# Kernel tuning notes

Hardware: AMD Instinct MI355X
Metric: run time of the kernel (lower is better)

The kernel has to match this reference:

```python
import math
import jax, jax.numpy as jnp
import numpy as np

B, V, D, H, DE, DFF = 2, 2048, 1024, 16, 256, 4096
DK = D // H


def setup_inputs() -> dict:
    key = jax.random.key(0)
    ks = jax.random.split(key, 24)
    n = lambda k, shape, s=0.02: (jax.random.normal(k, shape, jnp.float32) * s)
    z = lambda *shape: jnp.zeros(shape, jnp.float32)
    return {
        'x': jax.random.normal(ks[0], (B, V, D), jnp.float32),
        'e_node': jax.random.normal(ks[1], (B, V, DE), jnp.float32),
        'conn': jax.random.uniform(ks[2], (B, V, V), jnp.float32),
        'ln1_g': jnp.ones((D,), jnp.float32), 'ln1_b': z(D),
        'f1w1': n(ks[3], (DE, 2 * D)), 'f1b1': z(2 * D),
        'f1w2': n(ks[4], (2 * D, 2 * D)), 'f1b2': z(2 * D),
        'wq': n(ks[5], (D, D)), 'bq': z(D),
        'wk': n(ks[6], (D, D)), 'bk': z(D),
        'wv': n(ks[7], (D, D)), 'bv': z(D),
        'wp': n(ks[8], (D, D)), 'bp': z(D),
        'ln2_g': jnp.ones((D,), jnp.float32), 'ln2_b': z(D),
        'f2w1': n(ks[9], (DE, 2 * D)), 'f2b1': z(2 * D),
        'f2w2': n(ks[10], (2 * D, 2 * D)), 'f2b2': z(2 * D),
        'ffw1': n(ks[11], (D, DFF)), 'ffb1': z(DFF),
        'ffw2': n(ks[12], (DFF, D)), 'ffb2': z(D),
    }


def _ln(x, g, b):
    m = x.mean(-1, keepdims=True)
    v = ((x - m) ** 2).mean(-1, keepdims=True)
    return (x - m) / jnp.sqrt(v + 1e-5) * g + b


def _film(e, w1, b1, w2, b2):
    h = jax.nn.gelu(e @ w1 + b1, approximate=False)  # torch F.gelu default = exact erf
    gb = h @ w2 + b2
    return jnp.split(gb, 2, axis=-1)  # gamma, beta


def reference(x, e_node, conn, ln1_g, ln1_b, f1w1, f1b1, f1w2, f1b2,
              wq, bq, wk, bk, wv, bv, wp, bp, ln2_g, ln2_b,
              f2w1, f2b1, f2w2, f2b2, ffw1, ffb1, ffw2, ffb2):
    b, v, d = x.shape
    # Pre-norm + FiLM 1
    y = _ln(x, ln1_g, ln1_b)
    g1, be1 = _film(e_node, f1w1, f1b1, f1w2, f1b2)
    y = y * (1.0 + g1) + be1
    # Multi-head attention with additive log(conn) mask
    heads = lambda t: t.reshape(b, v, H, DK).transpose(0, 2, 1, 3)  # [B,h,V,dk]
    Q = heads(y @ wq + bq)
    K = heads(y @ wk + bk)
    Vv = heads(y @ wv + bv)
    logits = jnp.einsum('bhqd,bhkd->bhqk', Q, K) / math.sqrt(DK)
    log_mask = jnp.log(jnp.clip(conn, 0.0, 1.0) + 1e-6)[:, None]  # [B,1,V,V]
    s = logits + log_mask
    s = s - s.max(-1, keepdims=True)
    a = jnp.exp(s)
    a = a / (a.sum(-1, keepdims=True) + 1e-8)
    o = jnp.einsum('bhqk,bhkd->bhqd', a, Vv)
    o = o.transpose(0, 2, 1, 3).reshape(b, v, d)
    x = x + (o @ wp + bp)
    # Pre-norm + FiLM 2 + FFN
    y2 = _ln(x, ln2_g, ln2_b)
    g2, be2 = _film(e_node, f2w1, f2b1, f2w2, f2b2)
    y2 = y2 * (1.0 + g2) + be2
    y2 = jax.nn.gelu(y2 @ ffw1 + ffb1, approximate=False) @ ffw2 + ffb2
    return x + y2
```

## Files before the change

### kernel.cpp

```cpp
#include <hip/hip_runtime.h>
#include <math.h>
#include <stdint.h>

#define B_   2
#define V_   2048
#define D_   1024
#define H_   16
#define DK_  64
#define DE_  256
#define DFF_ 4096
#define M_   (B_*V_)
#define D2_  (2*D_)
#define D3_  (3*D_)

typedef unsigned short u16;
typedef unsigned int   u32;
typedef __bf16 bf16x8 __attribute__((ext_vector_type(8)));
typedef u16    u16x8  __attribute__((ext_vector_type(8)));
typedef u16    u16x4  __attribute__((ext_vector_type(4)));
typedef float  f32x4  __attribute__((ext_vector_type(4)));
typedef u32    u32x2  __attribute__((ext_vector_type(2)));
typedef u32    u32x4  __attribute__((ext_vector_type(4)));

__device__ __forceinline__ float bf2f(u16 u) {
    union { unsigned int i; float f; } z; z.i = ((unsigned int)u) << 16; return z.f;
}
__device__ __forceinline__ u16 f2bf(float f) {
    union { float f; unsigned int i; } z; z.f = f;
    unsigned int x = z.i;
    return (u16)((x + 0x7fffu + ((x >> 16) & 1u)) >> 16);
}
__device__ __forceinline__ float gelu_erf(float v) {
    return 0.5f * v * (1.0f + erff(v * 0.70710678118654752f));
}
__device__ __forceinline__ float ldv(const float* p) { return *p; }
__device__ __forceinline__ float ldv(const u16* p)   { return bf2f(*p); }
__device__ __forceinline__ void  stv(float* p, float v) { *p = v; }
__device__ __forceinline__ void  stv(u16* p,   float v) { *p = f2bf(v); }

__device__ __forceinline__ void gload16(const u16* g, u16* lds)
{
    __builtin_amdgcn_global_load_lds(
        (const __attribute__((address_space(1))) void*)g,
        (__attribute__((address_space(3))) void*)(uintptr_t)lds,
        16, 0, 0);
}

__global__ void convT_k(const float* __restrict__ W, u16* __restrict__ Wt, int K, int N)
{
    __shared__ float tile[32][33];
    const int n0 = blockIdx.x * 32, k0 = blockIdx.y * 32;
    const int tx = threadIdx.x, ty = threadIdx.y;
    #pragma unroll
    for (int j = 0; j < 4; ++j)
        tile[ty * 4 + j][tx] = W[(size_t)(k0 + ty * 4 + j) * N + n0 + tx];
    __syncthreads();
    #pragma unroll
    for (int j = 0; j < 4; ++j)
        Wt[(size_t)(n0 + ty * 4 + j) * K + k0 + tx] = f2bf(tile[tx][ty * 4 + j]);
}

__global__ void conv_k(const float* __restrict__ X, u16* __restrict__ Y)
{
    const int i = (blockIdx.x * 256 + threadIdx.x) * 4;
    f32x4 v = *reinterpret_cast<const f32x4*>(X + i);
    u16x4 o;
    #pragma unroll
    for (int j = 0; j < 4; ++j) o[j] = f2bf(v[j]);
    *reinterpret_cast<u16x4*>(Y + i) = o;
}

__global__ void lmask_k(const float* __restrict__ conn, u16* __restrict__ Lm)
{
    const size_t i = ((size_t)blockIdx.x * 256 + threadIdx.x) * 8;
    f32x4 a = *reinterpret_cast<const f32x4*>(conn + i);
    f32x4 b = *reinterpret_cast<const f32x4*>(conn + i + 4);
    u16x8 o;
    #pragma unroll
    for (int j = 0; j < 4; ++j) {
        o[j]     = f2bf(__log2f(fminf(fmaxf(a[j], 0.f), 1.f) + 1e-6f));
        o[j + 4] = f2bf(__log2f(fminf(fmaxf(b[j], 0.f), 1.f) + 1e-6f));
    }
    *reinterpret_cast<u16x8*>(Lm + i) = o;
}

__global__ void qkvbias_k(const float* __restrict__ bq, const float* __restrict__ bk,
                          const float* __restrict__ bv, float* __restrict__ o)
{
    int i = blockIdx.x * 256 + threadIdx.x;
    o[i] = i < 1024 ? bq[i] : (i < 2048 ? bk[i - 1024] : bv[i - 2048]);
}

template<int EPI, int BN, typename TC, typename TRES>
__launch_bounds__(256)
__global__ void gemm_k(const u16* __restrict__ A, const u16* __restrict__ Wt,
                       const float* __restrict__ bias, const TRES* __restrict__ res,
                       TC* __restrict__ C, int M, int N, int K)
{
    constexpr int NB = BN / 32;
    constexpr int IB = BN / 32;
    __shared__ u16 As[128 * 64];
    __shared__ u16 Bs[BN * 64];

    const int tid  = threadIdx.x;
    const int lane = tid & 63;
    const int w    = tid >> 6;
    const int wm   = (w >> 1) * 64, wn = (w & 1) * (BN / 2);
    const int m0   = blockIdx.y * 128, n0 = blockIdx.x * BN;
    const int l15  = lane & 15, l4 = lane >> 4;
    const int rStage = lane >> 3;

    int rrA[4], ccA[4];
    #pragma unroll
    for (int i = 0; i < 4; ++i) {
        rrA[i] = w * 32 + i * 8 + rStage;
        ccA[i] = (lane & 7) ^ (rrA[i] & 7);
    }
    int rrB[IB], ccB[IB];
    #pragma unroll
    for (int i = 0; i < IB; ++i) {
        rrB[i] = w * (BN / 4) + i * 8 + rStage;
        ccB[i] = (lane & 7) ^ (rrB[i] & 7);
    }

    f32x4 acc[4][NB] = {};

    for (int k0 = 0; k0 < K; k0 += 64) {
        if (k0) __syncthreads();
        #pragma unroll
        for (int i = 0; i < 4; ++i)
            gload16(A + (size_t)(m0 + rrA[i]) * K + k0 + ccA[i] * 8, &As[w * 2048 + i * 512]);
        #pragma unroll
        for (int i = 0; i < IB; ++i)
            gload16(Wt + (size_t)(n0 + rrB[i]) * K + k0 + ccB[i] * 8, &Bs[w * (BN * 16) + i * 512]);
        __syncthreads();

        #pragma unroll
        for (int kk = 0; kk < 2; ++kk) {
            bf16x8 a[4], b[NB];
            #pragma unroll
            for (int mb = 0; mb < 4; ++mb) {
                int r  = wm + mb * 16 + l15;
                int ph = (kk * 4 + l4) ^ (r & 7);
                a[mb] = *reinterpret_cast<const bf16x8*>(&As[r * 64 + ph * 8]);
            }
            #pragma unroll
            for (int nb = 0; nb < NB; ++nb) {
                int r  = wn + nb * 16 + l15;
                int ph = (kk * 4 + l4) ^ (r & 7);
                b[nb] = *reinterpret_cast<const bf16x8*>(&Bs[r * 64 + ph * 8]);
            }
            #pragma unroll
            for (int mb = 0; mb < 4; ++mb)
                #pragma unroll
                for (int nb = 0; nb < NB; ++nb)
                    acc[mb][nb] = __builtin_amdgcn_mfma_f32_16x16x32_bf16(a[mb], b[nb], acc[mb][nb], 0, 0, 0);
        }
    }

    #pragma unroll
    for (int nb = 0; nb < NB; ++nb) {
        int col = n0 + wn + nb * 16 + l15;
        float bv = bias[col];
        #pragma unroll
        for (int mb = 0; mb < 4; ++mb) {
            #pragma unroll
            for (int i = 0; i < 4; ++i) {
                int row = m0 + wm + mb * 16 + l4 * 4 + i;
                float v = acc[mb][nb][i] + bv;
                if (EPI == 1) v = gelu_erf(v);
                if (EPI == 2) v += ldv(res + (size_t)row * N + col);
                stv(C + (size_t)row * N + col, v);
            }
        }
    }
}

template<int EPI, typename TC>
__launch_bounds__(512, 2)
__global__ void gemm256_k(const u16* __restrict__ A, const u16* __restrict__ Wt,
                          const float* __restrict__ bias,
                          TC* __restrict__ C, int M, int N, int K)
{
    __shared__ u16 As[2][256 * 64];
    __shared__ u16 Bs[2][256 * 64];

    const int tid  = threadIdx.x;
    const int lane = tid & 63;
    const int w    = tid >> 6;
    const int wm   = (w >> 2) * 128;
    const int wn   = (w & 3) * 64;
    const int m0   = blockIdx.y * 256, n0 = blockIdx.x * 256;
    const int l15  = lane & 15, l4 = lane >> 4;

    int rr[4], cc[4];
    #pragma unroll
    for (int i = 0; i < 4; ++i) {
        rr[i] = i * 64 + w * 8 + (lane >> 3);
        cc[i] = (lane & 7) ^ (rr[i] & 7);
    }

    f32x4 acc[8][4] = {};
    const int NT = K / 64;

    #pragma unroll
    for (int i = 0; i < 4; ++i) {
        gload16(A  + (size_t)(m0 + rr[i]) * K + cc[i] * 8, &As[0][i * 4096 + w * 512]);
        gload16(Wt + (size_t)(n0 + rr[i]) * K + cc[i] * 8, &Bs[0][i * 4096 + w * 512]);
    }

    for (int t = 0; t < NT; ++t) {
        const int d = t & 1;
        __syncthreads();

        if (t + 1 < NT) {
            const int k1 = (t + 1) * 64;
            #pragma unroll
            for (int i = 0; i < 4; ++i) {
                gload16(A  + (size_t)(m0 + rr[i]) * K + k1 + cc[i] * 8, &As[d ^ 1][i * 4096 + w * 512]);
                gload16(Wt + (size_t)(n0 + rr[i]) * K + k1 + cc[i] * 8, &Bs[d ^ 1][i * 4096 + w * 512]);
            }
        }

        #pragma unroll
        for (int ph = 0; ph < 4; ++ph) {
            const int mh = ph >> 1, nh = ph & 1;
            bf16x8 a[4][2], b[2][2];
            #pragma unroll
            for (int mf = 0; mf < 4; ++mf)
                #pragma unroll
                for (int kk = 0; kk < 2; ++kk) {
                    int r  = wm + (mh * 4 + mf) * 16 + l15;
                    int p2 = (kk * 4 + l4) ^ (r & 7);
                    a[mf][kk] = *reinterpret_cast<const bf16x8*>(&As[d][r * 64 + p2 * 8]);
                }
            #pragma unroll
            for (int nf = 0; nf < 2; ++nf)
                #pragma unroll
                for (int kk = 0; kk < 2; ++kk) {
                    int r  = wn + (nh * 2 + nf) * 16 + l15;
                    int p2 = (kk * 4 + l4) ^ (r & 7);
                    b[nf][kk] = *reinterpret_cast<const bf16x8*>(&Bs[d][r * 64 + p2 * 8]);
                }
            __builtin_amdgcn_s_setprio(1);
            #pragma unroll
            for (int mf = 0; mf < 4; ++mf)
                #pragma unroll
                for (int nf = 0; nf < 2; ++nf)
                    #pragma unroll
                    for (int kk = 0; kk < 2; ++kk)
                        acc[mh * 4 + mf][nh * 2 + nf] = __builtin_amdgcn_mfma_f32_16x16x32_bf16(
                            a[mf][kk], b[nf][kk], acc[mh * 4 + mf][nh * 2 + nf], 0, 0, 0);
            __builtin_amdgcn_s_setprio(0);
            __builtin_amdgcn_sched_barrier(0);
        }
    }

    #pragma unroll
    for (int nf = 0; nf < 4; ++nf) {
        int col = n0 + wn + nf * 16 + l15;
        float bv = bias[col];
        #pragma unroll
        for (int mf = 0; mf < 8; ++mf) {
            #pragma unroll
            for (int i = 0; i < 4; ++i) {
                int row = m0 + wm + mf * 16 + l4 * 4 + i;
                float v = acc[mf][nf][i] + bv;
                if (EPI == 1) v = gelu_erf(v);
                stv(C + (size_t)row * N + col, v);
            }
        }
    }
}

template<typename TX>
__launch_bounds__(256)
__global__ void lnfilm_k(const TX* __restrict__ X, const u16* __restrict__ GB,
                         const float* __restrict__ g, const float* __restrict__ bb,
                         u16* __restrict__ Y)
{
    const int row = blockIdx.x;
    const int tid = threadIdx.x;
    const int d0  = tid * 4;
    const TX* xr = X + (size_t)row * D_ + d0;
    float xs[4], s = 0.f, sq = 0.f;
    if constexpr (sizeof(TX) == 4) {
        f32x4 v4 = *reinterpret_cast<const f32x4*>(xr);
        #pragma unroll
        for (int j = 0; j < 4; ++j) { xs[j] = v4[j]; s += xs[j]; sq += xs[j] * xs[j]; }
    } else {
        u16x4 v4 = *reinterpret_cast<const u16x4*>(xr);
        #pragma unroll
        for (int j = 0; j < 4; ++j) { xs[j] = bf2f(v4[j]); s += xs[j]; sq += xs[j] * xs[j]; }
    }
    #pragma unroll
    for (int off = 32; off; off >>= 1) {
        s  += __shfl_xor(s, off);
        sq += __shfl_xor(sq, off);
    }
    __shared__ float rs[4], rq[4];
    const int w = tid >> 6;
    if ((tid & 63) == 0) { rs[w] = s; rq[w] = sq; }
    __syncthreads();
    s  = rs[0] + rs[1] + rs[2] + rs[3];
    sq = rq[0] + rq[1] + rq[2] + rq[3];
    const float mean = s * (1.0f / D_);
    const float var  = sq * (1.0f / D_) - mean * mean;
    const float rstd = rsqrtf(fmaxf(var, 0.f) + 1e-5f);
    const u16* gbr = GB + (size_t)row * D2_ + d0;
    u16x4 g4 = *reinterpret_cast<const u16x4*>(gbr);
    u16x4 b4 = *reinterpret_cast<const u16x4*>(gbr + D_);
    f32x4 gg = *reinterpret_cast<const f32x4*>(g + d0);
    f32x4 bv = *reinterpret_cast<const f32x4*>(bb + d0);
    u16x4 o;
    #pragma unroll
    for (int j = 0; j < 4; ++j) {
        float v = (xs[j] - mean) * rstd * gg[j] + bv[j];
        v = v * (1.0f + bf2f(g4[j])) + bf2f(b4[j]);
        o[j] = f2bf(v);
    }
    *reinterpret_cast<u16x4*>(Y + (size_t)row * D_ + d0) = o;
}

__launch_bounds__(256)
__global__ void attn_k(const u16* __restrict__ Q, const u16* __restrict__ K,
                       const u16* __restrict__ Vv, const u16* __restrict__ Lm,
                       u16* __restrict__ O, int ld)
{
    __shared__ u16 Ks[64 * 64];
    __shared__ u16 Vs[64 * 64];
    __shared__ u16 Lms[128 * 64];
    __shared__ u16 Ps[128 * 72];

    const int blk = blockIdx.x;
    const int qt  = blk & 15;
    const int h   = (blk >> 4) & 15;
    const int b   = blk >> 8;
    const int q0  = qt * 128;
    const int tid = threadIdx.x, lane = tid & 63, w = tid >> 6;
    const int l15 = lane & 15, l4 = lane >> 4;
    const size_t bV = (size_t)b * V_;

    bf16x8 qa[2][2];
    #pragma unroll
    for (int g = 0; g < 2; ++g) {
        const u16* qp = Q + (bV + q0 + w * 32 + g * 16 + l15) * ld + h * 64;
        u16x8 r0 = *reinterpret_cast<const u16x8*>(qp + l4 * 8);
        u16x8 r1 = *reinterpret_cast<const u16x8*>(qp + 32 + l4 * 8);
        u16x8 s0, s1;
        #pragma unroll
        for (int j = 0; j < 8; ++j) {
            s0[j] = f2bf(bf2f(r0[j]) * 0.125f);
            s1[j] = f2bf(bf2f(r1[j]) * 0.125f);
        }
        union { u16x8 u; bf16x8 h; } c0, c1;
        c0.u = s0; c1.u = s1;
        qa[g][0] = c0.h; qa[g][1] = c1.h;
    }

    const int rStage = (lane >> 3);
    const int cSw    = ((lane & 7) ^ rStage) * 8;
    const int vK     = ((lane >> 5) << 2) + ((lane & 7) >> 1);
    const int vDk    = ((lane >> 3) & 3) * 16 + (lane & 1) * 8;
    const u32 vaddr  = (u32)(uintptr_t)&Vs[0] + (l4 << 10) + (l15 << 3);

    int lmOff[4];
    #pragma unroll
    for (int kb = 0; kb < 4; ++kb)
        lmOff[kb] = ((((kb << 1) | (l4 >> 1)) ^ (l15 & 7)) << 3);

    const float LOG2E = 1.44269504088896f;
    float lrp[2] = {0.f, 0.f};
    f32x4 o4[2][4] = {};

    for (int kt = 0; kt < V_ / 64; ++kt) {
        const int k0 = kt * 64;
        if (kt) __syncthreads();
        #pragma unroll
        for (int i = 0; i < 2; ++i) {
            int r  = i * 32 + w * 8 + rStage;
            int kv = i * 32 + w * 8 + vK;
            gload16(K  + (bV + k0 + r)  * ld + h * 64 + cSw, &Ks[i * 2048 + w * 512]);
            gload16(Vv + (bV + k0 + kv) * ld + h * 64 + vDk, &Vs[i * 2048 + w * 512]);
        }
        #pragma unroll
        for (int i = 0; i < 4; ++i) {
            int r = i * 32 + w * 8 + rStage;
            gload16(Lm + (bV + q0 + r) * (size_t)V_ + k0 + cSw, &Lms[i * 2048 + w * 512]);
        }
        __syncthreads();

        #pragma unroll
        for (int g = 0; g < 2; ++g) {
            f32x4 s[4];
            #pragma unroll
            for (int kb = 0; kb < 4; ++kb) {
                int row = (kb * 16 + l15) * 64;
                bf16x8 k0f = *reinterpret_cast<const bf16x8*>(&Ks[row + ((l4 ^ (l15 & 7)) * 8)]);
                bf16x8 k1f = *reinterpret_cast<const bf16x8*>(&Ks[row + (((l4 + 4) ^ (l15 & 7)) * 8)]);
                f32x4 z = {};
                __builtin_amdgcn_s_setprio(1);
                z = __builtin_amdgcn_mfma_f32_16x16x32_bf16(k0f, qa[g][0], z, 0, 0, 0);
                z = __builtin_amdgcn_mfma_f32_16x16x32_bf16(k1f, qa[g][1], z, 0, 0, 0);
                __builtin_amdgcn_s_setprio(0);
                s[kb] = z;
            }
            const int lmRow = w * 32 + g * 16 + l15;
            const u16* lmBase = &Lms[lmRow * 64 + (l4 & 1) * 4];
            u16* psW = &Ps[lmRow * 72 + l4 * 4];
            #pragma unroll
            for (int kb = 0; kb < 4; ++kb) {
                u16x4 lm4 = *reinterpret_cast<const u16x4*>(lmBase + lmOff[kb]);
                float p0, p1, p2, p3;
                float t0 = fmaf(s[kb][0], LOG2E, bf2f(lm4[0]));
                float t1 = fmaf(s[kb][1], LOG2E, bf2f(lm4[1]));
                float t2 = fmaf(s[kb][2], LOG2E, bf2f(lm4[2]));
                float t3 = fmaf(s[kb][3], LOG2E, bf2f(lm4[3]));
                asm("v_exp_f32 %0, %1" : "=v"(p0) : "v"(t0));
                asm("v_exp_f32 %0, %1" : "=v"(p1) : "v"(t1));
                asm("v_exp_f32 %0, %1" : "=v"(p2) : "v"(t2));
                asm("v_exp_f32 %0, %1" : "=v"(p3) : "v"(t3));
                lrp[g] += (p0 + p1) + (p2 + p3);
                u32 d0, d1;
                asm("v_cvt_pk_bf16_f32 %0, %1, %2" : "=v"(d0) : "v"(p0), "v"(p1));
                asm("v_cvt_pk_bf16_f32 %0, %1, %2" : "=v"(d1) : "v"(p2), "v"(p3));
                u32x2 dd = {d0, d1};
                *reinterpret_cast<u32x2*>(psW + kb * 16) = dd;
            }
        }

        union VU { u32x4 u; bf16x8 h; };
        VU vb[2][4];
        #pragma unroll
        for (int c2 = 0; c2 < 2; ++c2) {
            u32 a0 = vaddr + c2 * 4096;
            u32x2 t0, t1, t2, t3, t4, t5, t6, t7;
            asm volatile("ds_read_b64_tr_b16 %0, %1"            : "=v"(t0) : "v"(a0));
            asm volatile("ds_read_b64_tr_b16 %0, %1 offset:512" : "=v"(t1) : "v"(a0));
            asm volatile("ds_read_b64_tr_b16 %0, %1 offset:128" : "=v"(t2) : "v"(a0));
            asm volatile("ds_read_b64_tr_b16 %0, %1 offset:640" : "=v"(t3) : "v"(a0));
            asm volatile("ds_read_b64_tr_b16 %0, %1 offset:256" : "=v"(t4) : "v"(a0));
            asm volatile("ds_read_b64_tr_b16 %0, %1 offset:768" : "=v"(t5) : "v"(a0));
            asm volatile("ds_read_b64_tr_b16 %0, %1 offset:384" : "=v"(t6) : "v"(a0));
            asm volatile("ds_read_b64_tr_b16 %0, %1 offset:896" : "=v"(t7) : "v"(a0));
            asm volatile("s_waitcnt lgkmcnt(0)" ::: "memory");
            __builtin_amdgcn_sched_barrier(0);
            vb[c2][0].u = (u32x4){t0.x, t0.y, t1.x, t1.y};
            vb[c2][1].u = (u32x4){t2.x, t2.y, t3.x, t3.y};
            vb[c2][2].u = (u32x4){t4.x, t4.y, t5.x, t5.y};
            vb[c2][3].u = (u32x4){t6.x, t6.y, t7.x, t7.y};
        }
        #pragma unroll
        for (int g = 0; g < 2; ++g) {
            const u16* pr = &Ps[(w * 32 + g * 16 + l15) * 72];
            bf16x8 pa0 = *reinterpret_cast<const bf16x8*>(pr + l4 * 8);
            bf16x8 pa1 = *reinterpret_cast<const bf16x8*>(pr + 32 + l4 * 8);
            __builtin_amdgcn_s_setprio(1);
            #pragma unroll
            for (int nb = 0; nb < 4; ++nb) {
                o4[g][nb] = __builtin_amdgcn_mfma_f32_16x16x32_bf16(pa0, vb[0][nb].h, o4[g][nb], 0, 0, 0);
                o4[g][nb] = __builtin_amdgcn_mfma_f32_16x16x32_bf16(pa1, vb[1][nb].h, o4[g][nb], 0, 0, 0);
            }
            __builtin_amdgcn_s_setprio(0);
        }
    }

    #pragma unroll
    for (int g = 0; g < 2; ++g) {
        float v = lrp[g];
        v += __shfl_xor(v, 16);
        v += __shfl_xor(v, 32);
        #pragma unroll
        for (int i = 0; i < 4; ++i) {
            float lw = __shfl(v, (lane & 48) | ((l4 << 2) + i));
            float rcp = 1.0f / (lw + 1e-8f);
            int q = q0 + w * 32 + g * 16 + l4 * 4 + i;
            u16* op = O + (bV + q) * D_ + h * 64;
            #pragma unroll
            for (int nb = 0; nb < 4; ++nb)
                op[nb * 16 + l15] = f2bf(o4[g][nb][i] * rcp);
        }
    }
}

extern "C" void kernel_launch(void* const* d_in, const int* in_sizes, int n_in,
                              void* d_out, int out_size, void* d_ws, size_t ws_size,
                              hipStream_t stream)
{
    (void)in_sizes; (void)n_in; (void)out_size; (void)ws_size;
    const float* x    = (const float*)d_in[0];
    const float* e    = (const float*)d_in[1];
    const float* conn = (const float*)d_in[2];
    const float* ln1g = (const float*)d_in[3];
    const float* ln1b = (const float*)d_in[4];
    const float* f1w1 = (const float*)d_in[5];
    const float* f1b1 = (const float*)d_in[6];
    const float* f1w2 = (const float*)d_in[7];
    const float* f1b2 = (const float*)d_in[8];
    const float* wq   = (const float*)d_in[9];
    const float* bq   = (const float*)d_in[10];
    const float* wk   = (const float*)d_in[11];
    const float* bk   = (const float*)d_in[12];
    const float* wv   = (const float*)d_in[13];
    const float* bv   = (const float*)d_in[14];
    const float* wp   = (const float*)d_in[15];
    const float* bp   = (const float*)d_in[16];
    const float* ln2g = (const float*)d_in[17];
    const float* ln2b = (const float*)d_in[18];
    const float* f2w1 = (const float*)d_in[19];
    const float* f2b1 = (const float*)d_in[20];
    const float* f2w2 = (const float*)d_in[21];
    const float* f2b2 = (const float*)d_in[22];
    const float* ffw1 = (const float*)d_in[23];
    const float* ffb1 = (const float*)d_in[24];
    const float* ffw2 = (const float*)d_in[25];
    const float* ffb2 = (const float*)d_in[26];
    float* out = (float*)d_out;

    char* ws = (char*)d_ws;
    const size_t MB = 1u << 20;
    u16*   Lm    = (u16*)(ws + 0);
    u16*   e_bf  = (u16*)(ws + 16 * MB);
    u16*   h     = (u16*)(ws + 18 * MB);
    u16*   wt2   = (u16*)(ws + 34 * MB);
    u16*   wt8   = (u16*)(ws + 36 * MB);
    u16*   gb    = (u16*)(ws + 44 * MB);
    u16*   y     = (u16*)(ws + 60 * MB);
    u16*   wqkvt = (u16*)(ws + 18 * MB);
    u16*   qkv   = (u16*)(ws + 24 * MB);
    float* qkvb  = (float*)(ws + 71 * MB);
    u16*   o     = (u16*)(ws + 48 * MB);
    u16*   xnew  = (u16*)(ws + 64 * MB);
    u16*   h2    = (u16*)(ws + 18 * MB);
    u16*   gb2   = (u16*)(ws + 44 * MB);
    u16*   y2    = (u16*)(ws + 0);
    u16*   ffw1t = (u16*)(ws + 8 * MB);
    u16*   t     = (u16*)(ws + 16 * MB);
    u16*   ffw2t = (u16*)(ws + 48 * MB);

    dim3 blk(256), blk512(512), tblk(32, 8);
    #define CONVT(W, WT, K, N) convT_k<<<dim3((N)/32, (K)/32), tblk, 0, stream>>>(W, WT, K, N)

    conv_k <<<(M_*DE_)/1024, blk, 0, stream>>>(e, e_bf);
    lmask_k<<<(B_*(size_t)V_*V_)/2048, blk, 0, stream>>>(conn, Lm);

    CONVT(f1w1, wt2, DE_, D2_);
    gemm_k<1, 64, u16, u16><<<dim3(D2_/64, M_/128), blk, 0, stream>>>(e_bf, wt2, f1b1, (const u16*)nullptr, h, M_, D2_, DE_);
    CONVT(f1w2, wt8, D2_, D2_);
    gemm_k<0, 64, u16, u16><<<dim3(D2_/64, M_/128), blk, 0, stream>>>(h, wt8, f1b2, (const u16*)nullptr, gb, M_, D2_, D2_);
    lnfilm_k<float><<<M_, blk, 0, stream>>>(x, gb, ln1g, ln1b, y);
    CONVT(wq, wqkvt,                 D_, D_);
    CONVT(wk, wqkvt + 1024 * 1024,   D_, D_);
    CONVT(wv, wqkvt + 2048 * 1024,   D_, D_);
    qkvbias_k<<<D3_/256, blk, 0, stream>>>(bq, bk, bv, qkvb);
    gemm256_k<0, u16><<<dim3(D3_/256, M_/256), blk512, 0, stream>>>(y, wqkvt, qkvb, qkv, M_, D3_, D_);
    attn_k<<<B_*H_*(V_/128), blk, 0, stream>>>(qkv, qkv + 1024, qkv + 2048, Lm, o, D3_);
    CONVT(wp, wt2, D_, D_);
    gemm_k<2, 64, u16, float><<<dim3(D_/64, M_/128), blk, 0, stream>>>(o, wt2, bp, x, xnew, M_, D_, D_);
    CONVT(f2w1, wt2, DE_, D2_);
    gemm_k<1, 64, u16, u16><<<dim3(D2_/64, M_/128), blk, 0, stream>>>(e_bf, wt2, f2b1, (const u16*)nullptr, h2, M_, D2_, DE_);
    CONVT(f2w2, wt8, D2_, D2_);
    gemm_k<0, 64, u16, u16><<<dim3(D2_/64, M_/128), blk, 0, stream>>>(h2, wt8, f2b2, (const u16*)nullptr, gb2, M_, D2_, D2_);
    lnfilm_k<u16><<<M_, blk, 0, stream>>>(xnew, gb2, ln2g, ln2b, y2);
    CONVT(ffw1, ffw1t, D_, DFF_);
    gemm256_k<1, u16><<<dim3(DFF_/256, M_/256), blk512, 0, stream>>>(y2, ffw1t, ffb1, t, M_, DFF_, D_);
    CONVT(ffw2, ffw2t, DFF_, D_);
    gemm_k<2, 64, float, u16><<<dim3(D_/64, M_/128), blk, 0, stream>>>(t, ffw2t, ffb2, xnew, out, M_, D_, DFF_);
    #undef CONVT
}
```

Baseline: 417.5 us.

## Double-buffer small GEMM tiles with partial vmcnt waits and raw barriers

The 128-row GEMM kernel moves from a single LDS buffer to two, so the next K tile's global-to-LDS loads are issued before the current tile is computed. Both GEMM kernels now use raw s_barrier with explicit partial vmcnt waits, so only the current tile must have landed while the prefetch stays in flight. The attention kernel also drops its s_setprio calls around the MFMA blocks. This doubles LDS use in the smaller GEMM, which may lower occupancy, and the hand-written vmcnt counts must match the number of loads issued per stage.

```diff
diff --git a/kernel.cpp b/kernel.cpp
--- a/kernel.cpp
+++ b/kernel.cpp
@@ -46,6 +46,13 @@
         16, 0, 0);
 }
 
+__device__ __forceinline__ void barrier_raw()
+{
+    asm volatile("" ::: "memory");
+    __builtin_amdgcn_s_barrier();
+    asm volatile("" ::: "memory");
+}
+
 __global__ void convT_k(const float* __restrict__ W, u16* __restrict__ Wt, int K, int N)
 {
     __shared__ float tile[32][33];
@@ -99,8 +106,8 @@
 {
     constexpr int NB = BN / 32;
     constexpr int IB = BN / 32;
-    __shared__ u16 As[128 * 64];
-    __shared__ u16 Bs[BN * 64];
+    __shared__ u16 As[2][128 * 64];
+    __shared__ u16 Bs[2][BN * 64];
 
     const int tid  = threadIdx.x;
     const int lane = tid & 63;
@@ -123,17 +130,33 @@
         ccB[i] = (lane & 7) ^ (rrB[i] & 7);
     }
 
+    auto stage = [&](int kt, int dd) {
+        const int k0 = kt * 64;
+        #pragma unroll
+        for (int i = 0; i < 4; ++i)
+            gload16(A + (size_t)(m0 + rrA[i]) * K + k0 + ccA[i] * 8, &As[dd][w * 2048 + i * 512]);
+        #pragma unroll
+        for (int i = 0; i < IB; ++i)
+            gload16(Wt + (size_t)(n0 + rrB[i]) * K + k0 + ccB[i] * 8, &Bs[dd][w * (BN * 16) + i * 512]);
+    };
+
     f32x4 acc[4][NB] = {};
-
-    for (int k0 = 0; k0 < K; k0 += 64) {
-        if (k0) __syncthreads();
-        #pragma unroll
-        for (int i = 0; i < 4; ++i)
-            gload16(A + (size_t)(m0 + rrA[i]) * K + k0 + ccA[i] * 8, &As[w * 2048 + i * 512]);
-        #pragma unroll
-        for (int i = 0; i < IB; ++i)
-            gload16(Wt + (size_t)(n0 + rrB[i]) * K + k0 + ccB[i] * 8, &Bs[w * (BN * 16) + i * 512]);
-        __syncthreads();
+    const int NT = K / 64;
+
+    stage(0, 0);
+
+    for (int t = 0; t < NT; ++t) {
+        const int d = t & 1;
+        barrier_raw();
+        if (t + 1 < NT) {
+            stage(t + 1, d ^ 1);
+            if constexpr (BN == 128) asm volatile("s_waitcnt vmcnt(8)" ::: "memory");
+            else                     asm volatile("s_waitcnt vmcnt(6)" ::: "memory");
+        } else {
+            asm volatile("s_waitcnt vmcnt(0)" ::: "memory");
+        }
+        barrier_raw();
+        __builtin_amdgcn_sched_barrier(0);
 
         #pragma unroll
         for (int kk = 0; kk < 2; ++kk) {
@@ -142,13 +165,13 @@
             for (int mb = 0; mb < 4; ++mb) {
                 int r  = wm + mb * 16 + l15;
                 int ph = (kk * 4 + l4) ^ (r & 7);
-                a[mb] = *reinterpret_cast<const bf16x8*>(&As[r * 64 + ph * 8]);
+                a[mb] = *reinterpret_cast<const bf16x8*>(&As[d][r * 64 + ph * 8]);
             }
             #pragma unroll
             for (int nb = 0; nb < NB; ++nb) {
                 int r  = wn + nb * 16 + l15;
                 int ph = (kk * 4 + l4) ^ (r & 7);
-                b[nb] = *reinterpret_cast<const bf16x8*>(&Bs[r * 64 + ph * 8]);
+                b[nb] = *reinterpret_cast<const bf16x8*>(&Bs[d][r * 64 + ph * 8]);
             }
             #pragma unroll
             for (int mb = 0; mb < 4; ++mb)
@@ -200,27 +223,31 @@
         cc[i] = (lane & 7) ^ (rr[i] & 7);
     }
 
+    auto stage = [&](int kt, int dd) {
+        const int k0 = kt * 64;
+        #pragma unroll
+        for (int i = 0; i < 4; ++i) {
+            gload16(A  + (size_t)(m0 + rr[i]) * K + k0 + cc[i] * 8, &As[dd][i * 4096 + w * 512]);
+            gload16(Wt + (size_t)(n0 + rr[i]) * K + k0 + cc[i] * 8, &Bs[dd][i * 4096 + w * 512]);
+        }
+    };
+
     f32x4 acc[8][4] = {};
     const int NT = K / 64;
 
-    #pragma unroll
-    for (int i = 0; i < 4; ++i) {
-        gload16(A  + (size_t)(m0 + rr[i]) * K + cc[i] * 8, &As[0][i * 4096 + w * 512]);
-        gload16(Wt + (size_t)(n0 + rr[i]) * K + cc[i] * 8, &Bs[0][i * 4096 + w * 512]);
-    }
+    stage(0, 0);
 
     for (int t = 0; t < NT; ++t) {
         const int d = t & 1;
-        __syncthreads();
-
+        barrier_raw();
         if (t + 1 < NT) {
-            const int k1 = (t + 1) * 64;
-            #pragma unroll
-            for (int i = 0; i < 4; ++i) {
-                gload16(A  + (size_t)(m0 + rr[i]) * K + k1 + cc[i] * 8, &As[d ^ 1][i * 4096 + w * 512]);
-                gload16(Wt + (size_t)(n0 + rr[i]) * K + k1 + cc[i] * 8, &Bs[d ^ 1][i * 4096 + w * 512]);
-            }
-        }
+            stage(t + 1, d ^ 1);
+            asm volatile("s_waitcnt vmcnt(8)" ::: "memory");
+        } else {
+            asm volatile("s_waitcnt vmcnt(0)" ::: "memory");
+        }
+        barrier_raw();
+        __builtin_amdgcn_sched_barrier(0);
 
         #pragma unroll
         for (int ph = 0; ph < 4; ++ph) {
@@ -399,10 +426,8 @@
                 bf16x8 k0f = *reinterpret_cast<const bf16x8*>(&Ks[row + ((l4 ^ (l15 & 7)) * 8)]);
                 bf16x8 k1f = *reinterpret_cast<const bf16x8*>(&Ks[row + (((l4 + 4) ^ (l15 & 7)) * 8)]);
                 f32x4 z = {};
-                __builtin_amdgcn_s_setprio(1);
                 z = __builtin_amdgcn_mfma_f32_16x16x32_bf16(k0f, qa[g][0], z, 0, 0, 0);
                 z = __builtin_amdgcn_mfma_f32_16x16x32_bf16(k1f, qa[g][1], z, 0, 0, 0);
-                __builtin_amdgcn_s_setprio(0);
                 s[kb] = z;
             }
             const int lmRow = w * 32 + g * 16 + l15;
@@ -455,13 +480,11 @@
             const u16* pr = &Ps[(w * 32 + g * 16 + l15) * 72];
             bf16x8 pa0 = *reinterpret_cast<const bf16x8*>(pr + l4 * 8);
             bf16x8 pa1 = *reinterpret_cast<const bf16x8*>(pr + 32 + l4 * 8);
-            __builtin_amdgcn_s_setprio(1);
             #pragma unroll
             for (int nb = 0; nb < 4; ++nb) {
                 o4[g][nb] = __builtin_amdgcn_mfma_f32_16x16x32_bf16(pa0, vb[0][nb].h, o4[g][nb], 0, 0, 0);
                 o4[g][nb] = __builtin_amdgcn_mfma_f32_16x16x32_bf16(pa1, vb[1][nb].h, o4[g][nb], 0, 0, 0);
             }
-            __builtin_amdgcn_s_setprio(0);
         }
     }
 
```

Result: no change. 410.7 us (-1.6%).
